# Performance work log

Hardware: AMD Instinct MI355X
Metric: run time of the kernel (lower is better)

The kernel has to match this reference:

```python
import jax, jax.numpy as jnp
import numpy as np

B, C, L, E = 32, 3, 512, 512


def setup_inputs() -> dict:
    key = jax.random.key(0)
    ks = jax.random.split(key, 13)
    bnd = float(np.sqrt(6.0 / (2.0 * E)))  # xavier-uniform-like bound
    uni = lambda k, shp: jax.random.uniform(k, shp, jnp.float32, -bnd, bnd)
    return {
        "A0": jax.random.normal(ks[0], (B, C, L, L), jnp.float32),
        "x0": jax.random.normal(ks[1], (B, C, L, E), jnp.float32),
        "u0": jax.random.normal(ks[2], (B, C, E), jnp.float32),
        "t0": jax.random.normal(ks[3], (B, E), jnp.float32),
        "t1": jax.random.normal(ks[4], (B, E), jnp.float32),
        "Q_weight": uni(ks[5], (C, E, E)),
        "Q_bias": jnp.zeros((C, E), jnp.float32),
        "V_weight": uni(ks[6], (C, E, E)),
        "V_bias": jnp.zeros((C, E), jnp.float32),
        "K_weight": uni(ks[7], (C, E, E)),
        "K_bias": jnp.zeros((C, E), jnp.float32),
        "T_weight": uni(ks[8], (C, E, E)),
        "T_bias": jnp.zeros((C, E), jnp.float32),
    }


def reference(A0, x0, u0, t0, t1,
              Q_weight, Q_bias, V_weight, V_bias,
              K_weight, K_bias, T_weight, T_bias):
    # Time embeddings: (B,E) @ (C,E,E) -> (B,C,E)
    T0 = jnp.einsum('be,cef->bcf', t0, T_weight)
    T1 = jnp.einsum('be,cef->bcf', t1, T_weight)

    # Original modulates weight columns: x @ (W * T) == (x @ W) * T (T broadcasts
    # over the input axis via unsqueeze(-2)); use the fused, equivalent form.
    Q = jnp.einsum('bce,cef->bcf', x0[:, :, -1, :], Q_weight) * T0 + Q_bias  # (B,C,E)
    K = jnp.einsum('bce,cef->bcf', u0, K_weight) * T1 + K_bias               # (B,C,E)
    V = jnp.einsum('bcle,cef->bclf', x0, V_weight) * T1[:, :, None, :] \
        + V_bias[None, :, None, :]                                           # (B,C,L,E)

    QKV = jax.nn.softmax(jnp.einsum('bce,bcle->bcl', Q * K, V), axis=-1)     # (B,C,L)

    # A1[:, :, i, :] = A0[:, :, i+1, :] - A0[:, :, 0, :] for i < L-1;
    # A1[:, :, L-1, :] = A1[:, :, L-2, :] + QKV  (= A0[-1] - A0[0] + QKV)
    rows = A0[:, :, 1:, :] - A0[:, :, :1, :]                                 # (B,C,L-1,L)
    last = rows[:, :, -1, :] + QKV                                           # (B,C,L)
    A1 = jnp.concatenate([rows, last[:, :, None, :]], axis=2)                # (B,C,L,L)

    x1 = jnp.einsum('bclm,bcme->bcle', A1, x0)                               # (B,C,L,E)
    x1 = jnp.diff(x1, axis=2, prepend=jnp.zeros_like(x1[:, :, :1, :]))

    num = jnp.sum(T0 * T1, axis=-1)                                          # (B,C)
    den = jnp.sqrt(jnp.sum(T0 * T0, axis=-1) + jnp.sum(T1 * T1, axis=-1))
    w = (num / den)[..., None]                                               # (B,C,1)

    u1 = u0 * (1.0 - w) + x1.mean(axis=-2) * w                               # (B,C,E)
    return (A1 - A0, x1 - x0, u1 - u0)
```

## Files before the change

kernel.cpp:

```cpp
#include <hip/hip_runtime.h>
#include <stdint.h>

#define BB 32
#define CC 3
#define LL 512
#define EE 512
#define NBC (BB*CC)

#define O2_OFF ((size_t)NBC*LL*LL)
#define O3_OFF (O2_OFF + (size_t)NBC*LL*EE)

#define WSB_QX    0
#define WSB_H     196608
#define WSB_W     442368
#define WSB_ADIFF ((size_t)512*1024)
#define ADIFF_BYTES ((size_t)NBC*LL*LL*2)
#define WSB_X0T   (WSB_ADIFF + ADIFF_BYTES)
#define WS_FAST_NEED (WSB_X0T + ADIFF_BYTES)

#define NEC 16

typedef short bf16x8 __attribute__((ext_vector_type(8)));
typedef float f32x4  __attribute__((ext_vector_type(4)));
typedef unsigned short u16x8 __attribute__((ext_vector_type(8)));

__device__ __forceinline__ float wred_sum(float v){
#pragma unroll
  for (int m = 32; m >= 1; m >>= 1) v += __shfl_xor(v, m, 64);
  return v;
}
__device__ __forceinline__ float wred_max(float v){
#pragma unroll
  for (int m = 32; m >= 1; m >>= 1) v = fmaxf(v, __shfl_xor(v, m, 64));
  return v;
}
__device__ __forceinline__ void f4ma(float4& a, float s, const float4& b){
  a.x = fmaf(s, b.x, a.x); a.y = fmaf(s, b.y, a.y);
  a.z = fmaf(s, b.z, a.z); a.w = fmaf(s, b.w, a.w);
}
__device__ __forceinline__ float4 f4sub(const float4& a, const float4& b){
  return make_float4(a.x-b.x, a.y-b.y, a.z-b.z, a.w-b.w);
}
__device__ __forceinline__ unsigned short f2bf(float x){
  unsigned u = __float_as_uint(x);
  return (unsigned short)((u + 0x7FFFu + ((u >> 16) & 1u)) >> 16);
}
__device__ __forceinline__ float bf2f(unsigned short h){
  return __uint_as_float(((unsigned)h) << 16);
}
__device__ __forceinline__ void split1(float v, unsigned short& hi, unsigned short& lo){
  hi = f2bf(v);
  lo = f2bf(v - bf2f(hi));
}
__device__ __forceinline__ void st_nt_f4(float* p, float4 v){
  f32x4 w; w[0]=v.x; w[1]=v.y; w[2]=v.z; w[3]=v.w;
  __builtin_nontemporal_store(w, reinterpret_cast<f32x4*>(p));
}
__device__ __forceinline__ void st_nt_f(float* p, float v){
  __builtin_nontemporal_store(v, p);
}

__global__ __launch_bounds__(512) void conv2m(
    const float* __restrict__ A0, const float* __restrict__ x0,
    const float* __restrict__ u0,
    const float* __restrict__ t0, const float* __restrict__ t1,
    const float* __restrict__ Qw, const float* __restrict__ Kw,
    const float* __restrict__ Tw,
    float* __restrict__ out1, char* __restrict__ adiff, char* __restrict__ x0t,
    float* __restrict__ P)
{
  const int bid = blockIdx.x;
  const int t = threadIdx.x;
  __shared__ float T[64][65];
  __shared__ float vb[4][4][32];

  if (bid < 768) {
    const int bc = bid >> 3, tile = bid & 7;
    const int r0 = tile*64;
    const size_t abase = (size_t)bc*LL*LL;
    char* ad = adiff + (size_t)bc*LL*LL*2;
    const int q4 = t & 127, rg = t >> 7;
    const int base = r0 + rg*16;
    const float4 z = *reinterpret_cast<const float4*>(A0 + abase + q4*4);
    float4 prev = *reinterpret_cast<const float4*>(A0 + abase + (size_t)base*LL + q4*4);
#pragma unroll 4
    for (int i = 0; i < 16; ++i) {
      int gr = base + i;
      float4 cur;
      if (gr + 1 < LL)
        cur = *reinterpret_cast<const float4*>(A0 + abase + (size_t)(gr+1)*LL + q4*4);
      else cur = prev;
      float4 d;
      if (gr < LL-1) {
        d = f4sub(cur, prev);
        st_nt_f4(out1 + abase + (size_t)gr*LL + q4*4, f4sub(d, z));
      } else {
        d = make_float4(0.f,0.f,0.f,0.f);
      }
      if ((gr >> 2) == q4) {
        int e = gr & 3;
        d.x -= (e == 0) ? 1.0f : 0.0f;
        d.y -= (e == 1) ? 1.0f : 0.0f;
        d.z -= (e == 2) ? 1.0f : 0.0f;
        d.w -= (e == 3) ? 1.0f : 0.0f;
      }
      ushort4 pk;
      pk.x = f2bf(d.x); pk.y = f2bf(d.y); pk.z = f2bf(d.z); pk.w = f2bf(d.w);
      *reinterpret_cast<ushort4*>(ad + (size_t)gr*1024 + q4*8) = pk;
      prev = cur;
    }
  } else if (bid < 1536) {
    const int bid1 = bid - 768;
    const int bc = bid1 >> 3, tile = bid1 & 7;
    const int m0 = tile*64;
    const size_t xbase = (size_t)bc*LL*EE;
    char* xt = x0t + (size_t)bc*LL*EE*2;
    u16x8 outs[8];
#pragma unroll
    for (int ech = 0; ech < 8; ++ech) {
      const int e0 = ech*64;
      {
        int ml = t >> 3, seg = t & 7;
        const float* src = x0 + xbase + (size_t)(m0+ml)*EE + e0 + seg*8;
        float4 v0 = *reinterpret_cast<const float4*>(src);
        float4 v1 = *reinterpret_cast<const float4*>(src+4);
        T[ml][seg*8+0]=v0.x; T[ml][seg*8+1]=v0.y; T[ml][seg*8+2]=v0.z; T[ml][seg*8+3]=v0.w;
        T[ml][seg*8+4]=v1.x; T[ml][seg*8+5]=v1.y; T[ml][seg*8+6]=v1.z; T[ml][seg*8+7]=v1.w;
      }
      __syncthreads();
      {
        int el = t >> 3, c3 = t & 7;
        int mb = c3*8;
        u16x8 p;
        p[0]=f2bf(T[mb+0][el]); p[1]=f2bf(T[mb+1][el]);
        p[2]=f2bf(T[mb+2][el]); p[3]=f2bf(T[mb+3][el]);
        p[4]=f2bf(T[mb+4][el]); p[5]=f2bf(T[mb+5][el]);
        p[6]=f2bf(T[mb+6][el]); p[7]=f2bf(T[mb+7][el]);
        outs[ech] = p;
      }
      __syncthreads();
    }
    {
      int el = t >> 3, c3 = t & 7;
#pragma unroll
      for (int ech = 0; ech < 8; ++ech) {
        int eg = ech*64 + el;
        *reinterpret_cast<u16x8*>(xt + (size_t)eg*1024 + (size_t)(m0 + c3*8)*2) = outs[ech];
      }
    }
  } else {
    const int idx = bid - 1536;
    const int bg = idx & 7;
    const int rem = idx >> 3;
    const int c  = rem % 3;
    const int ec = rem / 3;
    const int b0 = bg*4;
    const int e0 = ec*32;
    const int f  = t;
    {
      int vec = f >> 7, j = (f >> 5) & 3, e = f & 31;
      int bb = b0 + j;
      float v;
      if      (vec == 0) v = t0[bb*EE + e0 + e];
      else if (vec == 1) v = t1[bb*EE + e0 + e];
      else if (vec == 2) v = x0[((size_t)(bb*CC + c)*LL + (LL-1))*EE + e0 + e];
      else               v = u0[(size_t)(bb*CC + c)*EE + e0 + e];
      vb[vec][j][e] = v;
    }
    __syncthreads();
    const float* twp = Tw + (size_t)c*EE*EE + (size_t)e0*EE + f;
    const float* qwp = Qw + (size_t)c*EE*EE + (size_t)e0*EE + f;
    const float* kwp = Kw + (size_t)c*EE*EE + (size_t)e0*EE + f;
    float aT0[4]={0,0,0,0}, aT1[4]={0,0,0,0}, aQ[4]={0,0,0,0}, aK[4]={0,0,0,0};
#pragma unroll 8
    for (int e = 0; e < 32; ++e) {
      float wt = twp[(size_t)e*EE];
      float wq = qwp[(size_t)e*EE];
      float wk = kwp[(size_t)e*EE];
#pragma unroll
      for (int j = 0; j < 4; ++j) {
        aT0[j] = fmaf(vb[0][j][e], wt, aT0[j]);
        aT1[j] = fmaf(vb[1][j][e], wt, aT1[j]);
        aQ[j]  = fmaf(vb[2][j][e], wq, aQ[j]);
        aK[j]  = fmaf(vb[3][j][e], wk, aK[j]);
      }
    }
#pragma unroll
    for (int j = 0; j < 4; ++j) {
      int cb = c*BB + b0 + j;
      P[(((size_t)0*NEC + ec)*96 + cb)*EE + f] = aT0[j];
      P[(((size_t)1*NEC + ec)*96 + cb)*EE + f] = aT1[j];
      P[(((size_t)2*NEC + ec)*96 + cb)*EE + f] = aQ[j];
      P[(((size_t)3*NEC + ec)*96 + cb)*EE + f] = aK[j];
    }
  }
}

__global__ __launch_bounds__(512) void k0c(
    const float* __restrict__ P,
    const float* __restrict__ Qb, const float* __restrict__ Kb,
    float* __restrict__ gtbuf, float* __restrict__ ws_w)
{
  const int bc = blockIdx.x;
  const int b = bc / CC, c = bc % CC;
  const int cb = c*BB + b;
  const int f = threadIdx.x;
  const int wid = f >> 6, lane = f & 63;
  __shared__ float red[8][3];
  float aT0=0.f, aT1=0.f, aQ=0.f, aK=0.f;
#pragma unroll
  for (int ec = 0; ec < NEC; ++ec) {
    aT0 += P[(((size_t)0*NEC + ec)*96 + cb)*EE + f];
    aT1 += P[(((size_t)1*NEC + ec)*96 + cb)*EE + f];
    aQ  += P[(((size_t)2*NEC + ec)*96 + cb)*EE + f];
    aK  += P[(((size_t)3*NEC + ec)*96 + cb)*EE + f];
  }
  float Qv = aQ*aT0 + Qb[c*EE + f];
  float Kv = aK*aT1 + Kb[c*EE + f];
  gtbuf[(size_t)cb*EE + f] = Qv*Kv*aT1;
  float pn = wred_sum(aT0*aT1);
  float p0 = wred_sum(aT0*aT0);
  float p1 = wred_sum(aT1*aT1);
  if (lane == 0) { red[wid][0]=pn; red[wid][1]=p0; red[wid][2]=p1; }
  __syncthreads();
  if (f == 0) {
    float sn=0.f, s0=0.f, s1=0.f;
    for (int i=0;i<8;++i){ sn+=red[i][0]; s0+=red[i][1]; s1+=red[i][2]; }
    ws_w[bc] = sn / sqrtf(s0 + s1);
  }
}

__global__ __launch_bounds__(256) void k1_h(
    const float* __restrict__ Vw, const float* __restrict__ gtbuf,
    float* __restrict__ ws_h)
{
  const int nt = blockIdx.x;
  const int c  = blockIdx.y;
  const int n0 = nt*128;
  const int t = threadIdx.x, lane = t & 63, w = t >> 6;
  __shared__ __align__(16) char AgtH[32*1024];
  __shared__ __align__(16) char AgtL[32*1024];
  __shared__ __align__(16) char BvH[128*128];
  __shared__ __align__(16) char BvL[128*128];
  {
    int row = t >> 3, sl = t & 7;
    const float* src = gtbuf + ((size_t)(c*BB + row))*EE + sl*64;
#pragma unroll
    for (int c3 = 0; c3 < 8; ++c3) {
      float4 a = *reinterpret_cast<const float4*>(src + c3*8);
      float4 b = *reinterpret_cast<const float4*>(src + c3*8 + 4);
      ushort4 h0,h1,l0,l1;
      split1(a.x,h0.x,l0.x); split1(a.y,h0.y,l0.y); split1(a.z,h0.z,l0.z); split1(a.w,h0.w,l0.w);
      split1(b.x,h1.x,l1.x); split1(b.y,h1.y,l1.y); split1(b.z,h1.z,l1.z); split1(b.w,h1.w,l1.w);
      int off = row*1024 + sl*128 + ((c3 ^ (row & 7)) << 4);
      *reinterpret_cast<ushort4*>(AgtH + off)     = h0;
      *reinterpret_cast<ushort4*>(AgtH + off + 8) = h1;
      *reinterpret_cast<ushort4*>(AgtL + off)     = l0;
      *reinterpret_cast<ushort4*>(AgtL + off + 8) = l1;
    }
  }
  f32x4 acc[2][2];
#pragma unroll
  for (int mi=0; mi<2; ++mi)
#pragma unroll
    for (int ni=0; ni<2; ++ni) acc[mi][ni] = (f32x4){0.f,0.f,0.f,0.f};

  for (int kk = 0; kk < 8; ++kk) {
    __syncthreads();
    {
      int nl = t >> 1, half = t & 1;
      const float* src = Vw + (size_t)c*EE*EE + (size_t)(n0+nl)*EE + kk*64 + half*32;
#pragma unroll
      for (int q = 0; q < 4; ++q) {
        float4 a = *reinterpret_cast<const float4*>(src + q*8);
        float4 b = *reinterpret_cast<const float4*>(src + q*8 + 4);
        int c3 = half*4 + q;
        ushort4 h0,h1,l0,l1;
        split1(a.x,h0.x,l0.x); split1(a.y,h0.y,l0.y); split1(a.z,h0.z,l0.z); split1(a.w,h0.w,l0.w);
        split1(b.x,h1.x,l1.x); split1(b.y,h1.y,l1.y); split1(b.z,h1.z,l1.z); split1(b.w,h1.w,l1.w);
        int off = nl*128 + ((c3 ^ (nl & 7)) << 4);
        *reinterpret_cast<ushort4*>(BvH + off)     = h0;
        *reinterpret_cast<ushort4*>(BvH + off + 8) = h1;
        *reinterpret_cast<ushort4*>(BvL + off)     = l0;
        *reinterpret_cast<ushort4*>(BvL + off + 8) = l1;
      }
    }
    __syncthreads();
    bf16x8 afH[2][2], afL[2][2], bfH[2][2], bfL[2][2];
#pragma unroll
    for (int mi=0; mi<2; ++mi)
#pragma unroll
      for (int ks=0; ks<2; ++ks) {
        int row = mi*16 + (lane & 15);
        int c3 = ks*4 + (lane >> 4);
        int off = row*1024 + kk*128 + ((c3 ^ (row & 7)) << 4);
        afH[mi][ks] = *reinterpret_cast<const bf16x8*>(AgtH + off);
        afL[mi][ks] = *reinterpret_cast<const bf16x8*>(AgtL + off);
      }
#pragma unroll
    for (int ni=0; ni<2; ++ni)
#pragma unroll
      for (int ks=0; ks<2; ++ks) {
        int n = w*32 + ni*16 + (lane & 15);
        int c3 = ks*4 + (lane >> 4);
        int off = n*128 + ((c3 ^ (n & 7)) << 4);
        bfH[ni][ks] = *reinterpret_cast<const bf16x8*>(BvH + off);
        bfL[ni][ks] = *reinterpret_cast<const bf16x8*>(BvL + off);
      }
#pragma unroll
    for (int mi=0; mi<2; ++mi)
#pragma unroll
      for (int ni=0; ni<2; ++ni)
#pragma unroll
        for (int ks=0; ks<2; ++ks) {
          acc[mi][ni] = __builtin_amdgcn_mfma_f32_16x16x32_bf16(afH[mi][ks], bfH[ni][ks], acc[mi][ni], 0, 0, 0);
          acc[mi][ni] = __builtin_amdgcn_mfma_f32_16x16x32_bf16(afH[mi][ks], bfL[ni][ks], acc[mi][ni], 0, 0, 0);
          acc[mi][ni] = __builtin_amdgcn_mfma_f32_16x16x32_bf16(afL[mi][ks], bfH[ni][ks], acc[mi][ni], 0, 0, 0);
        }
  }
#pragma unroll
  for (int mi=0; mi<2; ++mi)
#pragma unroll
    for (int ni=0; ni<2; ++ni)
#pragma unroll
      for (int r=0; r<4; ++r) {
        int b = mi*16 + (lane >> 4)*4 + r;
        int e = n0 + w*32 + ni*16 + (lane & 15);
        ws_h[((size_t)(b*CC + c))*EE + e] = acc[mi][ni][r];
      }
}

__global__ __launch_bounds__(512) void k2f(
    const float* __restrict__ A0, const float* __restrict__ x0,
    const float* __restrict__ u0,
    const float* __restrict__ ws_h, const float* __restrict__ ws_w,
    float* __restrict__ ws_qx, float* __restrict__ out1, float* __restrict__ out3)
{
  const int bc = blockIdx.x;
  const int tid = threadIdx.x, wid = tid >> 6, lane = tid & 63;
  __shared__ __align__(16) float hb[EE], sb[LL], a0r0[LL], a0r3[LL];
  __shared__ float red[8];
  __shared__ float partl[4][12][128];
  const size_t abase = (size_t)bc*LL*LL;
  const size_t xbase = (size_t)bc*LL*EE;
  hb[tid]   = ws_h[(size_t)bc*EE + tid];
  a0r0[tid] = A0[abase + tid];
  a0r3[tid] = A0[abase + (size_t)(LL-1)*LL + tid];
  __syncthreads();
  const float4 h0 = *reinterpret_cast<const float4*>(&hb[lane*8]);
  const float4 h1 = *reinterpret_cast<const float4*>(&hb[lane*8+4]);
  for (int l = wid; l < LL; l += 8) {
    const float4* xr = reinterpret_cast<const float4*>(x0 + xbase + (size_t)l*EE);
    float4 v0 = xr[lane*2], v1 = xr[lane*2+1];
    float acc = v0.x*h0.x + v0.y*h0.y + v0.z*h0.z + v0.w*h0.w
              + v1.x*h1.x + v1.y*h1.y + v1.z*h1.z + v1.w*h1.w;
    acc = wred_sum(acc);
    if (lane == 0) sb[l] = acc;
  }
  __syncthreads();
  float v = sb[tid];
  float mx = wred_max(v);
  if (lane == 0) red[wid] = mx;
  __syncthreads();
  mx = red[0];
#pragma unroll
  for (int i = 1; i < 8; ++i) mx = fmaxf(mx, red[i]);
  float ev = __expf(v - mx);
  float sm = wred_sum(ev);
  __syncthreads();
  if (lane == 0) red[wid] = sm;
  __syncthreads();
  float tot = 0.f;
#pragma unroll
  for (int i = 0; i < 8; ++i) tot += red[i];
  float qk = ev / tot;
  sb[tid] = qk;
  st_nt_f(out1 + abase + (size_t)(LL-1)*LL + tid, qk - a0r0[tid]);
  __syncthreads();
  const int mg = tid >> 7, cg = tid & 127;
  float4 aq = make_float4(0,0,0,0), a0s = make_float4(0,0,0,0), a3s = make_float4(0,0,0,0);
#pragma unroll 4
  for (int i = 0; i < 128; ++i) {
    int m = mg*128 + i;
    float4 xv = *reinterpret_cast<const float4*>(x0 + xbase + (size_t)m*EE + cg*4);
    float qm = sb[m], z0 = a0r0[m], z3 = a0r3[m];
    f4ma(aq, qm, xv); f4ma(a0s, z0, xv); f4ma(a3s, z3, xv);
  }
#pragma unroll
  for (int k = 0; k < 4; ++k) {
    partl[mg][0+k][cg] = (&aq.x)[k];
    partl[mg][4+k][cg] = (&a0s.x)[k];
    partl[mg][8+k][cg] = (&a3s.x)[k];
  }
  __syncthreads();
  if (mg == 0) {
    float wv = ws_w[bc];
    float4 uv = *reinterpret_cast<const float4*>(u0 + (size_t)bc*EE + cg*4);
    float4 qx4, o3;
#pragma unroll
    for (int k = 0; k < 4; ++k) {
      float q = 0.f, y0 = 0.f, y3 = 0.f;
#pragma unroll
      for (int g = 0; g < 4; ++g) {
        q  += partl[g][0+k][cg];
        y0 += partl[g][4+k][cg];
        y3 += partl[g][8+k][cg];
      }
      (&qx4.x)[k] = q;
      (&o3.x)[k] = wv * ((y3 - y0 + q) * (1.f/(float)LL) - (&uv.x)[k]);
    }
    *reinterpret_cast<float4*>(ws_qx + (size_t)bc*EE + cg*4) = qx4;
    st_nt_f4(out3 + (size_t)bc*EE + cg*4, o3);
  }
}

#define ASTR 80
__global__ __launch_bounds__(256) void k3_bf(
    const char* __restrict__ adiff, const char* __restrict__ x0t,
    const float* __restrict__ ws_qx, float* __restrict__ out2)
{
  const int bc = blockIdx.y;
  const int rt = blockIdx.x >> 2, nt = blockIdx.x & 3;
  const int r0 = rt*128, n0b = nt*128;
  const int t = threadIdx.x;
  const int lane = t & 63, wid = t >> 6;
  const int wr = wid >> 1, wc = wid & 1;
  __shared__ __align__(16) char As[128*ASTR];
  __shared__ __align__(16) char Bs[128*ASTR];
  const char* ad = adiff + (size_t)bc*LL*LL*2;
  const char* xt = x0t  + (size_t)bc*LL*EE*2;
  const size_t xbase = (size_t)bc*LL*EE;
  f32x4 acc[4][4];
#pragma unroll
  for (int mi=0; mi<4; ++mi)
#pragma unroll
    for (int ni=0; ni<4; ++ni) acc[mi][ni] = (f32x4){0.f,0.f,0.f,0.f};

  for (int k0 = 0; k0 < LL; k0 += 32) {
    __syncthreads();
#pragma unroll
    for (int i = 0; i < 2; ++i) {
      int idx = i*256 + t;
      int row = idx >> 2, c = idx & 3;
      int4 v = *reinterpret_cast<const int4*>(ad + (size_t)(r0+row)*1024 + k0*2 + c*16);
      *reinterpret_cast<int4*>(As + row*ASTR + c*16) = v;
    }
#pragma unroll
    for (int i = 0; i < 2; ++i) {
      int idx = i*256 + t;
      int n = idx >> 2, c = idx & 3;
      int4 v = *reinterpret_cast<const int4*>(xt + (size_t)(n0b+n)*1024 + k0*2 + c*16);
      int kb = (c*16) ^ (((n >> 2) & 3) << 4);
      *reinterpret_cast<int4*>(Bs + n*ASTR + kb) = v;
    }
    __syncthreads();
    bf16x8 af[4], bfv[4];
#pragma unroll
    for (int mi=0; mi<4; ++mi) {
      int row = wr*64 + mi*16 + (lane & 15);
      af[mi] = *reinterpret_cast<const bf16x8*>(As + row*ASTR + ((lane>>4)*16));
    }
#pragma unroll
    for (int ni=0; ni<4; ++ni) {
      int n = wc*64 + ni*16 + (lane & 15);
      int kb = ((lane>>4)*16) ^ (((n >> 2) & 3) << 4);
      bfv[ni] = *reinterpret_cast<const bf16x8*>(Bs + n*ASTR + kb);
    }
#pragma unroll
    for (int mi=0; mi<4; ++mi)
#pragma unroll
      for (int ni=0; ni<4; ++ni)
        acc[mi][ni] = __builtin_amdgcn_mfma_f32_16x16x32_bf16(af[mi], bfv[ni], acc[mi][ni], 0, 0, 0);
  }
#pragma unroll
  for (int mi=0; mi<4; ++mi)
#pragma unroll
    for (int r=0; r<4; ++r) {
      int grow = r0 + wr*64 + mi*16 + (lane>>4)*4 + r;
      const size_t rowoff = xbase + (size_t)grow*EE;
#pragma unroll
      for (int ni=0; ni<4; ++ni) {
        int gcol = n0b + wc*64 + ni*16 + (lane & 15);
        float val = acc[mi][ni][r];
        if (grow == LL-1) val += ws_qx[(size_t)bc*EE + gcol];
        st_nt_f(out2 + rowoff + gcol, val);
      }
    }
}

__global__ __launch_bounds__(512) void kA_fused(
    const float* __restrict__ A0, const float* __restrict__ x0,
    const float* __restrict__ u0,
    const float* __restrict__ t0, const float* __restrict__ t1,
    const float* __restrict__ Qw, const float* __restrict__ Qb,
    const float* __restrict__ Vw,
    const float* __restrict__ Kw, const float* __restrict__ Kb,
    const float* __restrict__ Tw,
    float* __restrict__ ws_qx, float* __restrict__ out1, float* __restrict__ out3)
{
  const int bc = blockIdx.x;
  const int b = bc / CC, c = bc % CC;
  const int tid = threadIdx.x;
  const int wid = tid >> 6, lane = tid & 63;
  __shared__ __align__(16) float t0v[EE], t1v[EE], xl[EE], uv[EE], gt[EE];
  __shared__ __align__(16) float hb[EE], sb[LL], a0r0[LL], a0r3[LL];
  __shared__ float red[3][8];
  __shared__ float wsh;
  const size_t abase = (size_t)bc*LL*LL;
  const size_t xbase = (size_t)bc*LL*EE;

  t0v[tid] = t0[b*EE + tid];
  t1v[tid] = t1[b*EE + tid];
  xl[tid]  = x0[xbase + (size_t)(LL-1)*EE + tid];
  uv[tid]  = u0[(size_t)bc*EE + tid];
  a0r0[tid] = A0[abase + tid];
  a0r3[tid] = A0[abase + (size_t)(LL-1)*LL + tid];
  __syncthreads();

  const int f = tid;
  const float* twp = Tw + (size_t)c*EE*EE + f;
  const float* qwp = Qw + (size_t)c*EE*EE + f;
  const float* kwp = Kw + (size_t)c*EE*EE + f;
  float aT0 = 0.f, aT1 = 0.f, aQ = 0.f, aK = 0.f;
  for (int e = 0; e < EE; ++e) {
    float wt = twp[(size_t)e*EE];
    aT0 = fmaf(t0v[e], wt, aT0);
    aT1 = fmaf(t1v[e], wt, aT1);
    aQ  = fmaf(xl[e],  qwp[(size_t)e*EE], aQ);
    aK  = fmaf(uv[e],  kwp[(size_t)e*EE], aK);
  }
  float Qv = aQ*aT0 + Qb[c*EE + f];
  float Kv = aK*aT1 + Kb[c*EE + f];
  gt[f] = Qv*Kv*aT1;

  float pn = wred_sum(aT0*aT1);
  float p0 = wred_sum(aT0*aT0);
  float p1 = wred_sum(aT1*aT1);
  if (lane == 0) { red[0][wid]=pn; red[1][wid]=p0; red[2][wid]=p1; }
  __syncthreads();
  if (tid == 0) {
    float sn=0.f, s0=0.f, s1=0.f;
    for (int i=0;i<8;++i){ sn+=red[0][i]; s0+=red[1][i]; s1+=red[2][i]; }
    wsh = sn / sqrtf(s0 + s1);
  }
  {
    const float4 g0 = *reinterpret_cast<const float4*>(&gt[lane*8]);
    const float4 g1 = *reinterpret_cast<const float4*>(&gt[lane*8+4]);
    for (int r = wid; r < EE; r += 8) {
      const float4* vr = reinterpret_cast<const float4*>(Vw + ((size_t)c*EE + r)*EE);
      float4 v0 = vr[lane*2], v1 = vr[lane*2+1];
      float acc = v0.x*g0.x + v0.y*g0.y + v0.z*g0.z + v0.w*g0.w
                + v1.x*g1.x + v1.y*g1.y + v1.z*g1.z + v1.w*g1.w;
      acc = wred_sum(acc);
      if (lane == 0) hb[r] = acc;
    }
  }
  __syncthreads();

  {
    const float4 h0 = *reinterpret_cast<const float4*>(&hb[lane*8]);
    const float4 h1 = *reinterpret_cast<const float4*>(&hb[lane*8+4]);
    for (int l = wid; l < LL; l += 8) {
      const float4* xr = reinterpret_cast<const float4*>(x0 + xbase + (size_t)l*EE);
      float4 v0 = xr[lane*2], v1 = xr[lane*2+1];
      float acc = v0.x*h0.x + v0.y*h0.y + v0.z*h0.z + v0.w*h0.w
                + v1.x*h1.x + v1.y*h1.y + v1.z*h1.z + v1.w*h1.w;
      acc = wred_sum(acc);
      if (lane == 0) sb[l] = acc;
    }
  }
  __syncthreads();

  float v = sb[tid];
  float mx = wred_max(v);
  if (lane == 0) red[0][wid] = mx;
  __syncthreads();
  mx = red[0][0];
#pragma unroll
  for (int i = 1; i < 8; ++i) mx = fmaxf(mx, red[0][i]);
  float ev = __expf(v - mx);
  float sm = wred_sum(ev);
  __syncthreads();
  if (lane == 0) red[0][wid] = sm;
  __syncthreads();
  float tot = 0.f;
#pragma unroll
  for (int i = 0; i < 8; ++i) tot += red[0][i];
  float qk = ev / tot;
  sb[tid] = qk;
  out1[abase + (size_t)(LL-1)*LL + tid] = qk - a0r0[tid];
  __syncthreads();

  float qx=0.f, y0=0.f, y3=0.f;
  for (int m = 0; m < LL; ++m) {
    float xm = x0[xbase + (size_t)m*EE + tid];
    qx = fmaf(sb[m],   xm, qx);
    y0 = fmaf(a0r0[m], xm, y0);
    y3 = fmaf(a0r3[m], xm, y3);
  }
  ws_qx[(size_t)bc*EE + tid] = qx;
  float mean = (y3 - y0 + qx) * (1.f/(float)LL);
  out3[(size_t)bc*EE + tid] = wsh * (mean - uv[tid]);
}

__global__ __launch_bounds__(256) void k3_mfma(
    const float* __restrict__ A0, const float* __restrict__ x0,
    const float* __restrict__ ws_qx,
    float* __restrict__ out1, float* __restrict__ out2)
{
  const int bc = blockIdx.y;
  const int rt = blockIdx.x >> 2, nt = blockIdx.x & 3;
  const int r0 = rt*128, n0b = nt*128;
  const int t = threadIdx.x;
  const int lane = t & 63, wid = t >> 6;
  const int wr = wid >> 1, wc = wid & 1;
  __shared__ __align__(16) char As[128*ASTR];
  __shared__ __align__(16) char Bs[128*ASTR];
  const size_t abase = (size_t)bc*LL*LL;
  const size_t xbase = (size_t)bc*LL*EE;
  f32x4 acc[4][4];
#pragma unroll
  for (int mi=0; mi<4; ++mi)
#pragma unroll
    for (int ni=0; ni<4; ++ni) acc[mi][ni] = (f32x4){0.f,0.f,0.f,0.f};
  const int bkl = (t & 7) * 4;
  const int bn0 = (t >> 3) * 4;
  for (int k0 = 0; k0 < LL; k0 += 32) {
    __syncthreads();
#pragma unroll
    for (int i = 0; i < 4; ++i) {
      int idx = i*256 + t;
      int row = idx >> 3, kq = idx & 7;
      int gr = r0 + row;
      int gr1 = (gr+1 > LL-1) ? (LL-1) : (gr+1);
      float4 va = *reinterpret_cast<const float4*>(A0 + abase + (size_t)gr *LL + k0 + kq*4);
      float4 vb = *reinterpret_cast<const float4*>(A0 + abase + (size_t)gr1*LL + k0 + kq*4);
      ushort4 pk;
      pk.x = f2bf(vb.x - va.x); pk.y = f2bf(vb.y - va.y);
      pk.z = f2bf(vb.z - va.z); pk.w = f2bf(vb.w - va.w);
      *reinterpret_cast<ushort4*>(As + row*ASTR + kq*8) = pk;
      if (nt == 0 && gr < LL-1) {
        float4 az = *reinterpret_cast<const float4*>(A0 + abase + k0 + kq*4);
        float4 o = make_float4(vb.x - az.x - va.x, vb.y - az.y - va.y,
                               vb.z - az.z - va.z, vb.w - az.w - va.w);
        *reinterpret_cast<float4*>(out1 + abase + (size_t)gr*LL + k0 + kq*4) = o;
      }
    }
    {
      float xq[4][4];
#pragma unroll
      for (int i = 0; i < 4; ++i)
        *reinterpret_cast<float4*>(xq[i]) =
          *reinterpret_cast<const float4*>(x0 + xbase + (size_t)(k0+bkl+i)*EE + n0b + bn0);
#pragma unroll
      for (int j = 0; j < 4; ++j) {
        int n = bn0 + j;
        ushort4 pk;
        pk.x = f2bf(xq[0][j]); pk.y = f2bf(xq[1][j]);
        pk.z = f2bf(xq[2][j]); pk.w = f2bf(xq[3][j]);
        int kb = (bkl*2) ^ (((n >> 2) & 3) << 4);
        *reinterpret_cast<ushort4*>(Bs + n*ASTR + kb) = pk;
      }
    }
    __syncthreads();
    bf16x8 af[4], bfv[4];
#pragma unroll
    for (int mi=0; mi<4; ++mi) {
      int row = wr*64 + mi*16 + (lane & 15);
      af[mi] = *reinterpret_cast<const bf16x8*>(As + row*ASTR + ((lane>>4)*16));
    }
#pragma unroll
    for (int ni=0; ni<4; ++ni) {
      int n = wc*64 + ni*16 + (lane & 15);
      int kb = ((lane>>4)*16) ^ (((n >> 2) & 3) << 4);
      bfv[ni] = *reinterpret_cast<const bf16x8*>(Bs + n*ASTR + kb);
    }
#pragma unroll
    for (int mi=0; mi<4; ++mi)
#pragma unroll
      for (int ni=0; ni<4; ++ni)
        acc[mi][ni] = __builtin_amdgcn_mfma_f32_16x16x32_bf16(af[mi], bfv[ni], acc[mi][ni], 0, 0, 0);
  }
#pragma unroll
  for (int mi=0; mi<4; ++mi)
#pragma unroll
    for (int r=0; r<4; ++r) {
      int grow = r0 + wr*64 + mi*16 + (lane>>4)*4 + r;
      const size_t rowoff = xbase + (size_t)grow*EE;
#pragma unroll
      for (int ni=0; ni<4; ++ni) {
        int gcol = n0b + wc*64 + ni*16 + (lane & 15);
        float xv = x0[rowoff + gcol];
        float val;
        if (grow == LL-1) val = ws_qx[(size_t)bc*EE + gcol] - xv;
        else              val = acc[mi][ni][r] - xv;
        out2[rowoff + gcol] = val;
      }
    }
}

extern "C" void kernel_launch(void* const* d_in, const int* in_sizes, int n_in,
                              void* d_out, int out_size, void* d_ws, size_t ws_size,
                              hipStream_t stream)
{
  const float* A0 = (const float*)d_in[0];
  const float* x0 = (const float*)d_in[1];
  const float* u0 = (const float*)d_in[2];
  const float* t0 = (const float*)d_in[3];
  const float* t1 = (const float*)d_in[4];
  const float* Qw = (const float*)d_in[5];
  const float* Qb = (const float*)d_in[6];
  const float* Vw = (const float*)d_in[7];
  const float* Kw = (const float*)d_in[9];
  const float* Kb = (const float*)d_in[10];
  const float* Tw = (const float*)d_in[11];

  char*  wsb    = (char*)d_ws;
  float* ws_qx  = (float*)(wsb + WSB_QX);
  float* ws_h   = (float*)(wsb + WSB_H);
  float* ws_w   = (float*)(wsb + WSB_W);

  float* out1 = (float*)d_out;
  float* out2 = out1 + O2_OFF;
  float* out3 = out1 + O3_OFF;
  float* gtbuf = out3;
  float* pscr  = out2;

  const bool fast = ws_size >= WS_FAST_NEED;

  if (fast) {
    char* adiff = wsb + WSB_ADIFF;
    char* x0t   = wsb + WSB_X0T;
    conv2m<<<1920, 512, 0, stream>>>(A0, x0, u0, t0, t1, Qw, Kw, Tw,
                                     out1, adiff, x0t, pscr);
    k0c<<<NBC, 512, 0, stream>>>(pscr, Qb, Kb, gtbuf, ws_w);
    k1_h<<<dim3(4, 3), 256, 0, stream>>>(Vw, gtbuf, ws_h);
    k2f<<<NBC, 512, 0, stream>>>(A0, x0, u0, ws_h, ws_w, ws_qx, out1, out3);
    k3_bf<<<dim3(16, NBC), 256, 0, stream>>>(adiff, x0t, ws_qx, out2);
  } else {
    kA_fused<<<NBC, 512, 0, stream>>>(A0, x0, u0, t0, t1, Qw, Qb, Vw, Kw, Kb, Tw,
                                      ws_qx, out1, out3);
    k3_mfma<<<dim3(16, NBC), 256, 0, stream>>>(A0, x0, ws_qx, out1, out2);
  }
}
```

Before: 238.4 us.

## Move A1-A0 output store from conv kernel into k3_bf GEMM loop

Measured after the change: 259.0 us. 8.7% more time.

```diff
diff --git a/kernel.cpp b/kernel.cpp
--- a/kernel.cpp
+++ b/kernel.cpp
@@ -66,7 +66,7 @@
     const float* __restrict__ t0, const float* __restrict__ t1,
     const float* __restrict__ Qw, const float* __restrict__ Kw,
     const float* __restrict__ Tw,
-    float* __restrict__ out1, char* __restrict__ adiff, char* __restrict__ x0t,
+    char* __restrict__ adiff, char* __restrict__ x0t,
     float* __restrict__ P)
 {
   const int bid = blockIdx.x;
@@ -81,7 +81,6 @@
     char* ad = adiff + (size_t)bc*LL*LL*2;
     const int q4 = t & 127, rg = t >> 7;
     const int base = r0 + rg*16;
-    const float4 z = *reinterpret_cast<const float4*>(A0 + abase + q4*4);
     float4 prev = *reinterpret_cast<const float4*>(A0 + abase + (size_t)base*LL + q4*4);
 #pragma unroll 4
     for (int i = 0; i < 16; ++i) {
@@ -91,12 +90,8 @@
         cur = *reinterpret_cast<const float4*>(A0 + abase + (size_t)(gr+1)*LL + q4*4);
       else cur = prev;
       float4 d;
-      if (gr < LL-1) {
-        d = f4sub(cur, prev);
-        st_nt_f4(out1 + abase + (size_t)gr*LL + q4*4, f4sub(d, z));
-      } else {
-        d = make_float4(0.f,0.f,0.f,0.f);
-      }
+      if (gr < LL-1) d = f4sub(cur, prev);
+      else           d = make_float4(0.f,0.f,0.f,0.f);
       if ((gr >> 2) == q4) {
         int e = gr & 3;
         d.x -= (e == 0) ? 1.0f : 0.0f;
@@ -417,7 +412,8 @@
 #define ASTR 80
 __global__ __launch_bounds__(256) void k3_bf(
     const char* __restrict__ adiff, const char* __restrict__ x0t,
-    const float* __restrict__ ws_qx, float* __restrict__ out2)
+    const float* __restrict__ A0, const float* __restrict__ ws_qx,
+    float* __restrict__ out1, float* __restrict__ out2)
 {
   const int bc = blockIdx.y;
   const int rt = blockIdx.x >> 2, nt = blockIdx.x & 3;
@@ -427,9 +423,14 @@
   const int wr = wid >> 1, wc = wid & 1;
   __shared__ __align__(16) char As[128*ASTR];
   __shared__ __align__(16) char Bs[128*ASTR];
+  __shared__ __align__(16) float zr[LL];
   const char* ad = adiff + (size_t)bc*LL*LL*2;
   const char* xt = x0t  + (size_t)bc*LL*EE*2;
+  const size_t abase = (size_t)bc*LL*LL;
   const size_t xbase = (size_t)bc*LL*EE;
+  const bool W1 = (nt == 0);
+  zr[t]       = A0[abase + t];
+  zr[t + 256] = A0[abase + t + 256];
   f32x4 acc[4][4];
 #pragma unroll
   for (int mi=0; mi<4; ++mi)
@@ -471,6 +472,27 @@
 #pragma unroll
       for (int ni=0; ni<4; ++ni)
         acc[mi][ni] = __builtin_amdgcn_mfma_f32_16x16x32_bf16(af[mi], bfv[ni], acc[mi][ni], 0, 0, 0);
+    if (W1) {
+      const int c4 = (t & 7) * 4;
+      const int gcol0 = k0 + c4;
+      const float4 zz = *reinterpret_cast<const float4*>(&zr[gcol0]);
+#pragma unroll
+      for (int rr = 0; rr < 4; ++rr) {
+        int row = rr*32 + (t >> 3);
+        int gr = r0 + row;
+        if (gr < LL-1) {
+          const unsigned short* ap = reinterpret_cast<const unsigned short*>(As + row*ASTR + c4*2);
+          float4 o;
+          o.x = bf2f(ap[0]); o.y = bf2f(ap[1]); o.z = bf2f(ap[2]); o.w = bf2f(ap[3]);
+          int e = gr - gcol0;
+          o.x += (e == 0) ? 1.0f : 0.0f;
+          o.y += (e == 1) ? 1.0f : 0.0f;
+          o.z += (e == 2) ? 1.0f : 0.0f;
+          o.w += (e == 3) ? 1.0f : 0.0f;
+          st_nt_f4(out1 + abase + (size_t)gr*LL + gcol0, f4sub(o, zz));
+        }
+      }
+    }
   }
 #pragma unroll
   for (int mi=0; mi<4; ++mi)
@@ -732,11 +754,11 @@
     char* adiff = wsb + WSB_ADIFF;
     char* x0t   = wsb + WSB_X0T;
     conv2m<<<1920, 512, 0, stream>>>(A0, x0, u0, t0, t1, Qw, Kw, Tw,
-                                     out1, adiff, x0t, pscr);
+                                     adiff, x0t, pscr);
     k0c<<<NBC, 512, 0, stream>>>(pscr, Qb, Kb, gtbuf, ws_w);
     k1_h<<<dim3(4, 3), 256, 0, stream>>>(Vw, gtbuf, ws_h);
     k2f<<<NBC, 512, 0, stream>>>(A0, x0, u0, ws_h, ws_w, ws_qx, out1, out3);
-    k3_bf<<<dim3(16, NBC), 256, 0, stream>>>(adiff, x0t, ws_qx, out2);
+    k3_bf<<<dim3(16, NBC), 256, 0, stream>>>(adiff, x0t, A0, ws_qx, out1, out2);
   } else {
     kA_fused<<<NBC, 512, 0, stream>>>(A0, x0, u0, t0, t1, Qw, Qb, Vw, Kw, Kb, Tw,
                                       ws_qx, out1, out3);
```
